# Optimization experiments

Measured on AMD Instinct MI355X. Metric: run time of the kernel, lower is better.

The kernel has to match this reference:

```python
import jax, jax.numpy as jnp
import numpy as np

B, S, DIM = 2, 2048, 2048
N_HEADS, N_KV_HEADS, HEAD_DIM = 16, 4, 128
ROPE_THETA = 10000.0
N_REP = N_HEADS // N_KV_HEADS


def make_freq_cis(seq_len, head_dim, theta):
    # (seq_len, head_dim//2, 2, 2) rotation matrices [[cos,-sin],[sin,cos]]
    freqs = 1.0 / (theta ** (np.arange(0, head_dim, 2, dtype=np.float32) / head_dim))
    t = np.arange(seq_len, dtype=np.float32)
    ang = np.outer(t, freqs)  # [S, head_dim//2]
    cos, sin = np.cos(ang), np.sin(ang)
    row0 = np.stack([cos, -sin], axis=-1)
    row1 = np.stack([sin, cos], axis=-1)
    return jnp.asarray(np.stack([row0, row1], axis=-2))  # [S, hd/2, 2, 2]


def setup_inputs() -> dict:
    key = jax.random.key(0)
    ks = jax.random.split(key, 5)
    std = DIM ** -0.5
    x = jax.random.normal(ks[0], (B, S, DIM), dtype=jnp.float32)
    wq = jax.random.normal(ks[1], (N_HEADS * HEAD_DIM, DIM), dtype=jnp.float32) * std
    wk = jax.random.normal(ks[2], (N_KV_HEADS * HEAD_DIM, DIM), dtype=jnp.float32) * std
    wv = jax.random.normal(ks[3], (N_KV_HEADS * HEAD_DIM, DIM), dtype=jnp.float32) * std
    wo = jax.random.normal(ks[4], (DIM, N_HEADS * HEAD_DIM), dtype=jnp.float32) * std
    freq_cis = make_freq_cis(S, HEAD_DIM, ROPE_THETA)
    return {"x": x, "freq_cis": freq_cis, "wq": wq, "wk": wk, "wv": wv, "wo": wo}


def apply_rotary(xh, fc):
    # xh: [B,S,H,hd]; fc: [S, hd/2, 2, 2]
    b, s, h, hd = xh.shape
    xr = xh.reshape(b, s, h, hd // 2, 2)
    out = jnp.einsum('bshdj,sdij->bshdi', xr, fc)
    return out.reshape(b, s, h, hd)


def attention_fwd(x, freq_cis, wq, wk, wv, wo):
    b, s, _ = x.shape
    xq = (x @ wq.T).reshape(b, s, N_HEADS, HEAD_DIM)
    xk = (x @ wk.T).reshape(b, s, N_KV_HEADS, HEAD_DIM)
    xv = (x @ wv.T).reshape(b, s, N_KV_HEADS, HEAD_DIM)
    xq = apply_rotary(xq, freq_cis[:s])
    xk = apply_rotary(xk, freq_cis[:s])
    # GQA repeat_kv (repeat_interleave along head dim)
    xk = jnp.repeat(xk, N_REP, axis=2)
    xv = jnp.repeat(xv, N_REP, axis=2)
    scale = HEAD_DIM ** -0.5
    scores = jnp.einsum('bqhd,bkhd->bhqk', xq, xk) * scale
    causal = jnp.tril(jnp.ones((s, s), dtype=bool))
    scores = jnp.where(causal[None, None], scores, jnp.float32(-1e30))
    probs = jax.nn.softmax(scores, axis=-1)
    out = jnp.einsum('bhqk,bkhd->bqhd', probs, xv).reshape(b, s, N_HEADS * HEAD_DIM)
    return out @ wo.T


def reference(x, freq_cis, wq, wk, wv, wo):
    return attention_fwd(x, freq_cis, wq, wk, wv, wo)
```

## Files before the change

kernel.cpp:

```cpp
#include <hip/hip_runtime.h>

#define S_LEN 2048
#define N_B 2
#define N_H 16
#define N_KVH 4
#define HD 128
#define LDQ 2048
#define LDK 1024

typedef __bf16 bf16x8 __attribute__((ext_vector_type(8)));
typedef float f32x4 __attribute__((ext_vector_type(4)));
typedef float f32x16 __attribute__((ext_vector_type(16)));
typedef int v2i __attribute__((ext_vector_type(2)));

__device__ __forceinline__ float bf2f(unsigned short u){
  unsigned int x = ((unsigned int)u) << 16; float f;
  __builtin_memcpy(&f, &x, 4); return f;
}
__device__ __forceinline__ unsigned short f2bf(float f){
  unsigned int x; __builtin_memcpy(&x, &f, 4);
  unsigned int r = x + 0x7fff + ((x >> 16) & 1);
  return (unsigned short)(r >> 16);
}
__device__ __forceinline__ unsigned int cvt_pk_bf16(float lo, float hi){
  unsigned int u;
  asm("v_cvt_pk_bf16_f32 %0, %1, %2" : "=v"(u) : "v"(lo), "v"(hi));
  return u;
}
__device__ __forceinline__ void gload16(const void* g, void* l){
  __builtin_amdgcn_global_load_lds((const __attribute__((address_space(1))) void*)g,
                                   (__attribute__((address_space(3))) void*)l, 16, 0, 0);
}

__global__ void cast_all(const float* __restrict__ x,  const float* __restrict__ wq,
                         const float* __restrict__ wk, const float* __restrict__ wv,
                         const float* __restrict__ wo, unsigned short* __restrict__ xb,
                         unsigned short* __restrict__ wqb, unsigned short* __restrict__ wkb,
                         unsigned short* __restrict__ wvb, unsigned short* __restrict__ wob){
  int i = blockIdx.x * 256 + threadIdx.x;
  const float* in; unsigned short* out; int j;
  if (i < 1048576)      { in = x;  out = xb;  j = i; }
  else if (i < 1572864) { in = wq; out = wqb; j = i - 1048576; }
  else if (i < 1703936) { in = wk; out = wkb; j = i - 1572864; }
  else if (i < 1835008) { in = wv; out = wvb; j = i - 1703936; }
  else                  { in = wo; out = wob; j = i - 1835008; }
  const float4* p = (const float4*)in + (size_t)j * 2;
  float4 a = p[0], b = p[1];
  uint4 o;
  o.x = (unsigned)f2bf(a.x) | ((unsigned)f2bf(a.y) << 16);
  o.y = (unsigned)f2bf(a.z) | ((unsigned)f2bf(a.w) << 16);
  o.z = (unsigned)f2bf(b.x) | ((unsigned)f2bf(b.y) << 16);
  o.w = (unsigned)f2bf(b.z) | ((unsigned)f2bf(b.w) << 16);
  ((uint4*)out)[j] = o;
}

__global__ void rope_kernel(unsigned short* __restrict__ X, const float* __restrict__ FC,
                            int cpr_log2, int ld_log2, int n8){
  int i = blockIdx.x * 256 + threadIdx.x;
  if (i >= n8) return;
  int row = i >> cpr_log2;
  int col = (i & ((1 << cpr_log2) - 1)) << 3;
  size_t idx = ((size_t)row << ld_log2) + col;
  int s = row & (S_LEN - 1);
  int d = col & (HD - 1);
  uint4 v = *(const uint4*)(X + idx);
  unsigned short* pv = (unsigned short*)&v;
  const float4* f4 = (const float4*)FC + ((size_t)s * 64 + (d >> 1));
  uint4 ov; unsigned short* po = (unsigned short*)&ov;
#pragma unroll
  for (int p = 0; p < 4; p++){
    float4 f = f4[p];
    float e = bf2f(pv[2*p]), o = bf2f(pv[2*p+1]);
    po[2*p]   = f2bf(f.x * e + f.y * o);
    po[2*p+1] = f2bf(f.z * e + f.w * o);
  }
  *(uint4*)(X + idx) = ov;
}

__global__ void transpose_v(const unsigned short* __restrict__ V, unsigned short* __restrict__ Vt, int ld){
  __shared__ unsigned short tile[32][33];
  int t = threadIdx.x;
  int s0 = blockIdx.x * 32;
  int c0 = blockIdx.y * 32;
  int r = t >> 3, cg = (t & 7) * 4;
  uint2 in2 = *(const uint2*)(V + (size_t)(s0 + r) * ld + c0 + cg);
  unsigned short* pi = (unsigned short*)&in2;
  tile[r][cg+0] = pi[0]; tile[r][cg+1] = pi[1]; tile[r][cg+2] = pi[2]; tile[r][cg+3] = pi[3];
  __syncthreads();
  int b = s0 >> 11, sl = s0 & (S_LEN - 1);
  int kvh = c0 >> 7, dd0 = c0 & (HD - 1);
  int dd = t >> 3, sg = (t & 7) * 4;
  uint2 o2; unsigned short* po = (unsigned short*)&o2;
  po[0] = tile[sg+0][dd]; po[1] = tile[sg+1][dd]; po[2] = tile[sg+2][dd]; po[3] = tile[sg+3][dd];
  *(uint2*)(Vt + (size_t)((b * N_KVH + kvh) * HD + dd0 + dd) * S_LEN + sl + sg) = o2;
}

__device__ __forceinline__ void storeC(float* C, size_t idx, float v){ C[idx] = v; }
__device__ __forceinline__ void storeC(unsigned short* C, size_t idx, float v){ C[idx] = f2bf(v); }

template <typename OutT>
__global__ __launch_bounds__(256, 2) void gemm_nt(const unsigned short* __restrict__ A,
                                                  const unsigned short* __restrict__ Bm,
                                                  OutT* __restrict__ C,
                                                  int M, int N, int K, int nbn){
  extern __shared__ char smem[];
  char* sA = smem; char* sB = smem + 16384;
  int bid = blockIdx.x;
  bid = (bid & 7) * (gridDim.x >> 3) + (bid >> 3);
  int bn = bid % nbn, bm = bid / nbn;
  int row0 = bm * 128, col0 = bn * 128;
  int t = threadIdx.x; int w = t >> 6, l = t & 63;
  int lr = l & 15, lg = l >> 4;
  int srow = t >> 3;
  int sg = (t & 7) ^ (srow & 7);
  const unsigned short* agp = A + (size_t)(row0 + srow) * K + sg * 8;
  const unsigned short* bgp = Bm + (size_t)(col0 + srow) * K + sg * 8;
  int wr = w >> 1, wc = w & 1;
  f32x4 acc[4][4] = {};
  for (int k0 = 0; k0 < K; k0 += 64){
    __syncthreads();
#pragma unroll
    for (int i = 0; i < 4; i++){
      gload16(agp + (size_t)i * 32 * K + k0, sA + i * 4096 + w * 1024);
      gload16(bgp + (size_t)i * 32 * K + k0, sB + i * 4096 + w * 1024);
    }
    __syncthreads();
#pragma unroll
    for (int kk = 0; kk < 2; kk++){
      bf16x8 af[4], bfv[4];
#pragma unroll
      for (int m = 0; m < 4; m++){
        int row = wr * 64 + m * 16 + lr;
        int kg = kk * 4 + lg;
        af[m] = *(const bf16x8*)(sA + row * 128 + ((kg ^ (row & 7)) << 4));
      }
#pragma unroll
      for (int n = 0; n < 4; n++){
        int row = wc * 64 + n * 16 + lr;
        int kg = kk * 4 + lg;
        bfv[n] = *(const bf16x8*)(sB + row * 128 + ((kg ^ (row & 7)) << 4));
      }
#pragma unroll
      for (int m = 0; m < 4; m++)
#pragma unroll
        for (int n = 0; n < 4; n++)
          acc[m][n] = __builtin_amdgcn_mfma_f32_16x16x32_bf16(af[m], bfv[n], acc[m][n], 0, 0, 0);
    }
  }
#pragma unroll
  for (int m = 0; m < 4; m++)
#pragma unroll
    for (int n = 0; n < 4; n++)
#pragma unroll
      for (int r = 0; r < 4; r++){
        int rr = row0 + wr * 64 + m * 16 + lg * 4 + r;
        int cc = col0 + wc * 64 + n * 16 + lr;
        storeC(C, (size_t)rr * N + cc, acc[m][n][r]);
      }
}

template <typename OutT>
__global__ __launch_bounds__(512, 2) void gemm_tpl(const unsigned short* __restrict__ A,
                                                   const unsigned short* __restrict__ Bm,
                                                   OutT* __restrict__ C,
                                                   int M, int N, int K, int nbn){
  extern __shared__ char smem[];
  int bid = blockIdx.x;
  bid = (bid & 7) * (gridDim.x >> 3) + (bid >> 3);
  int bn = bid % nbn, bm = bid / nbn;
  int row0 = bm * 128, col0 = bn * 256;
  int t = threadIdx.x, w = t >> 6, l = t & 63;
  int lr = l & 15, lg = l >> 4;
  int wm = w >> 2, wn = w & 3;
  int srow = t >> 3;
  int sg = (t & 7) ^ (srow & 7);
  const unsigned short* agp = A + (size_t)(row0 + srow) * K + sg * 8;
  const unsigned short* bgp = Bm + (size_t)(col0 + srow) * K + sg * 8;
  int nk = K >> 6;
  f32x4 acc[4][4] = {};

#define TPL_STAGE(j, s) do {                                                   \
    char* base_ = smem + (s) * 49152;                                          \
    int k0_ = (j) << 6;                                                        \
    _Pragma("unroll")                                                          \
    for (int i_ = 0; i_ < 2; i_++)                                             \
      gload16(agp + (size_t)i_ * 64 * K + k0_, base_ + i_ * 8192 + w * 1024);  \
    _Pragma("unroll")                                                          \
    for (int i_ = 0; i_ < 4; i_++)                                             \
      gload16(bgp + (size_t)i_ * 64 * K + k0_, base_ + 16384 + i_ * 8192 + w * 1024); \
  } while(0)

  TPL_STAGE(0, 0);
  TPL_STAGE(1, 1);
  int slot = 0;
  for (int j = 0; j < nk; j++){
    if (j + 1 < nk) asm volatile("s_waitcnt vmcnt(6)" ::: "memory");
    else            asm volatile("s_waitcnt vmcnt(0)" ::: "memory");
    __builtin_amdgcn_s_barrier();
    asm volatile("" ::: "memory");
    char* sA = smem + slot * 49152;
    char* sB = sA + 16384;
    bf16x8 af[2][4], bf[2][4];
#pragma unroll
    for (int kk = 0; kk < 2; kk++){
#pragma unroll
      for (int m = 0; m < 4; m++){
        int row = wm * 64 + m * 16 + lr;
        int kg = kk * 4 + lg;
        af[kk][m] = *(const bf16x8*)(sA + row * 128 + ((kg ^ (row & 7)) << 4));
      }
#pragma unroll
      for (int n = 0; n < 4; n++){
        int row = wn * 64 + n * 16 + lr;
        int kg = kk * 4 + lg;
        bf[kk][n] = *(const bf16x8*)(sB + row * 128 + ((kg ^ (row & 7)) << 4));
      }
    }
    if (j + 2 < nk){
      int sn = slot + 2; if (sn >= 3) sn -= 3;
      TPL_STAGE(j + 2, sn);
    }
    __builtin_amdgcn_s_setprio(1);
#pragma unroll
    for (int kk = 0; kk < 2; kk++)
#pragma unroll
      for (int m = 0; m < 4; m++)
#pragma unroll
        for (int n = 0; n < 4; n++)
          acc[m][n] = __builtin_amdgcn_mfma_f32_16x16x32_bf16(af[kk][m], bf[kk][n], acc[m][n], 0, 0, 0);
    __builtin_amdgcn_s_setprio(0);
    slot++; if (slot == 3) slot = 0;
  }
#undef TPL_STAGE
#pragma unroll
  for (int m = 0; m < 4; m++)
#pragma unroll
    for (int n = 0; n < 4; n++)
#pragma unroll
      for (int r = 0; r < 4; r++){
        int rr = row0 + wm * 64 + m * 16 + lg * 4 + r;
        int cc = col0 + wn * 64 + n * 16 + lr;
        storeC(C, (size_t)rr * N + cc, acc[m][n][r]);
      }
}

__global__ __launch_bounds__(256, 2) void attn_fwd(const unsigned short* __restrict__ Q,
                                                   const unsigned short* __restrict__ Kb,
                                                   const unsigned short* __restrict__ Vt,
                                                   unsigned short* __restrict__ P0,
                                                   unsigned short* __restrict__ P1,
                                                   float2* __restrict__ ML){
  extern __shared__ char smem[];
  const float SOFT_C = 0.088388347648318447f * 1.4426950408889634f;
  const float THR_RAW = 62.0f;
  int bid = blockIdx.x;
  bid = ((bid & 7) << 6) | (bid >> 3);
  int slot = bid & 15, h = (bid >> 4) & 15, b = bid >> 8;
  int p = slot & 7, half = slot >> 3;
  int kvh = h >> 2;
  int t = threadIdx.x, w = t >> 6, l = t & 63;
  int lq = l & 31, lh = l >> 5;
  unsigned short* Pout = half ? P1 : P0;
  float2* mlb = ML + half * (N_B * S_LEN * N_H);

  int gA = (t & 15) ^ (t >> 4);
  const unsigned short* kgp = Kb + ((size_t)(b * S_LEN) + (t >> 4)) * LDK + kvh * HD + gA * 8;
  int gV = (t & 7) ^ ((t >> 3) & 7);
  const unsigned short* vgp = Vt + ((size_t)((b * N_KVH + kvh) * HD) + (t >> 3)) * S_LEN + gV * 8;

  for (int phase = 0; phase < 2; phase++){
    int qt = phase ? (15 - p) : p;
    int q_lane = qt * 128 + w * 32 + lq;
    const unsigned short* qbase = Q + ((size_t)(b * S_LEN + q_lane)) * LDQ + h * HD + lh * 8;
    bf16x8 qf[8];
#pragma unroll
    for (int ks = 0; ks < 8; ks++)
      qf[ks] = *(const bf16x8*)(qbase + ks * 16);

    f32x16 o_acc[4] = {};
    float m_run = -1e4f, l_run = 0.f;
    int t_begin = half ? (qt + 1) : 0;
    int t_end   = half ? (2 * qt + 2) : (qt + 1);

    int pk0 = t_begin * 64;
#pragma unroll
    for (int m = 0; m < 4; m++)
      gload16(kgp + (size_t)(pk0 + m * 16) * LDK, smem + m * 4096 + w * 1024);
#pragma unroll
    for (int i = 0; i < 4; i++)
      gload16(vgp + (size_t)i * 32 * S_LEN + pk0, smem + 16384 + i * 4096 + w * 1024);
    __syncthreads();

    int cur = 0;
    for (int tix = t_begin; tix < t_end; tix++){
      int k0 = tix * 64;
      char* sK = smem + (cur << 15);
      char* sV = sK + 16384;
      if (tix + 1 < t_end){
        char* nb = smem + ((cur ^ 1) << 15);
        int nk0 = k0 + 64;
#pragma unroll
        for (int m = 0; m < 4; m++)
          gload16(kgp + (size_t)(nk0 + m * 16) * LDK, nb + m * 4096 + w * 1024);
#pragma unroll
        for (int i = 0; i < 4; i++)
          gload16(vgp + (size_t)i * 32 * S_LEN + nk0, nb + 16384 + i * 4096 + w * 1024);
      }

      f32x16 sc[2] = {};
      __builtin_amdgcn_s_setprio(1);
#pragma unroll
      for (int ks = 0; ks < 8; ks++){
#pragma unroll
        for (int n = 0; n < 2; n++){
          int row = n * 32 + lq;
          int pg = (ks * 2 + lh) ^ (row & 15);
          bf16x8 kf = *(const bf16x8*)(sK + row * 256 + pg * 16);
          sc[n] = __builtin_amdgcn_mfma_f32_32x32x16_bf16(kf, qf[ks], sc[n], 0, 0, 0);
        }
      }
      __builtin_amdgcn_s_setprio(0);
      if (tix >= 2 * qt){
#pragma unroll
        for (int n = 0; n < 2; n++)
#pragma unroll
          for (int reg = 0; reg < 16; reg++){
            int kv = k0 + n * 32 + (reg & 3) + 8 * (reg >> 2) + 4 * lh;
            if (kv > q_lane) sc[n][reg] = -1e30f;
          }
      }
      float tmax = sc[0][0];
#pragma unroll
      for (int n = 0; n < 2; n++)
#pragma unroll
        for (int reg = 0; reg < 16; reg++) tmax = fmaxf(tmax, sc[n][reg]);
      tmax = fmaxf(tmax, __shfl_xor(tmax, 32));
      if (!__all(tmax - m_run <= THR_RAW)){
        float nm = fmaxf(m_run, tmax);
        float rs = exp2f((m_run - nm) * SOFT_C);
        m_run = nm;
        l_run *= rs;
#pragma unroll
        for (int n = 0; n < 4; n++)
#pragma unroll
          for (int j = 0; j < 16; j++) o_acc[n][j] *= rs;
      }
      float lsum = 0.f;
#pragma unroll
      for (int n = 0; n < 2; n++)
#pragma unroll
        for (int reg = 0; reg < 16; reg++){
          float pv = exp2f((sc[n][reg] - m_run) * SOFT_C);
          sc[n][reg] = pv;
          lsum += pv;
        }
      lsum += __shfl_xor(lsum, 32);
      l_run += lsum;

      bf16x8 pb[4];
#pragma unroll
      for (int ks = 0; ks < 4; ks++){
        int n = ks >> 1;
        int R0 = (2 * ks) & 3, R1 = (2 * ks + 1) & 3;
        unsigned int WA0 = cvt_pk_bf16(sc[n][4 * R0 + 0], sc[n][4 * R0 + 1]);
        unsigned int WA1 = cvt_pk_bf16(sc[n][4 * R0 + 2], sc[n][4 * R0 + 3]);
        unsigned int WB0 = cvt_pk_bf16(sc[n][4 * R1 + 0], sc[n][4 * R1 + 1]);
        unsigned int WB1 = cvt_pk_bf16(sc[n][4 * R1 + 2], sc[n][4 * R1 + 3]);
        v2i s0 = __builtin_amdgcn_permlane32_swap((int)WA0, (int)WB0, false, false);
        v2i s1 = __builtin_amdgcn_permlane32_swap((int)WA1, (int)WB1, false, false);
        unsigned int pu[4] = {(unsigned int)s0.x, (unsigned int)s1.x,
                              (unsigned int)s0.y, (unsigned int)s1.y};
        pb[ks] = *(bf16x8*)pu;
      }
      __builtin_amdgcn_s_setprio(1);
#pragma unroll
      for (int n = 0; n < 4; n++){
#pragma unroll
        for (int ks = 0; ks < 4; ks++){
          int row = n * 32 + lq;
          int pg = (ks * 2 + lh) ^ (row & 7);
          bf16x8 vf = *(const bf16x8*)(sV + row * 128 + pg * 16);
          o_acc[n] = __builtin_amdgcn_mfma_f32_32x32x16_bf16(vf, pb[ks], o_acc[n], 0, 0, 0);
        }
      }
      __builtin_amdgcn_s_setprio(0);
      __syncthreads();
      cur ^= 1;
    }
    unsigned short* ob = Pout + ((size_t)(b * S_LEN + q_lane)) * LDQ + h * HD + 4 * lh;
#pragma unroll
    for (int n = 0; n < 4; n++)
#pragma unroll
      for (int g = 0; g < 4; g++){
        unsigned int u0 = cvt_pk_bf16(o_acc[n][4 * g + 0], o_acc[n][4 * g + 1]);
        unsigned int u1 = cvt_pk_bf16(o_acc[n][4 * g + 2], o_acc[n][4 * g + 3]);
        uint2 o2; o2.x = u0; o2.y = u1;
        *(uint2*)(ob + n * 32 + g * 8) = o2;
      }
    if (lh == 0)
      mlb[(size_t)(b * S_LEN + q_lane) * N_H + h] = make_float2(m_run, l_run);
  }
}

__global__ void attn_merge(unsigned short* __restrict__ P0, const unsigned short* __restrict__ P1,
                           const float2* __restrict__ ML){
  const float SOFT_C = 0.088388347648318447f * 1.4426950408889634f;
  int tid = blockIdx.x * 256 + threadIdx.x;
  float2 a = ML[tid >> 4];
  float2 c = ML[(N_B * S_LEN * N_H) + (tid >> 4)];
  float m = fmaxf(a.x, c.x);
  float w0 = exp2f((a.x - m) * SOFT_C) * a.y;
  float w1 = exp2f((c.x - m) * SOFT_C) * c.y;
  float inv = 1.0f / (w0 + w1);
  float s0 = exp2f((a.x - m) * SOFT_C) * inv;
  float s1 = exp2f((c.x - m) * SOFT_C) * inv;
  uint4 u0 = *(const uint4*)(P0 + (size_t)tid * 8);
  uint4 u1 = *(const uint4*)(P1 + (size_t)tid * 8);
  unsigned short* q0 = (unsigned short*)&u0;
  unsigned short* q1 = (unsigned short*)&u1;
  uint4 o;
  unsigned int* po = (unsigned int*)&o;
#pragma unroll
  for (int j = 0; j < 4; j++){
    float lo = s0 * bf2f(q0[2*j])   + s1 * bf2f(q1[2*j]);
    float hi = s0 * bf2f(q0[2*j+1]) + s1 * bf2f(q1[2*j+1]);
    po[j] = cvt_pk_bf16(lo, hi);
  }
  *(uint4*)(P0 + (size_t)tid * 8) = o;
}

extern "C" void kernel_launch(void* const* d_in, const int* in_sizes, int n_in,
                              void* d_out, int out_size, void* d_ws, size_t ws_size,
                              hipStream_t stream) {
  const float* x  = (const float*)d_in[0];
  const float* fc = (const float*)d_in[1];
  const float* wq = (const float*)d_in[2];
  const float* wk = (const float*)d_in[3];
  const float* wv = (const float*)d_in[4];
  const float* wo = (const float*)d_in[5];
  float* out = (float*)d_out;

  char* ws = (char*)d_ws;
  unsigned short* xb  = (unsigned short*)(ws);
  unsigned short* wqb = (unsigned short*)(ws + 16777216);
  unsigned short* wkb = (unsigned short*)(ws + 25165824);
  unsigned short* wvb = (unsigned short*)(ws + 27262976);
  unsigned short* wob = (unsigned short*)(ws + 29360128);
  unsigned short* qb_ = (unsigned short*)(ws + 37748736);
  unsigned short* kvb = (unsigned short*)(ws + 54525952);
  unsigned short* vtb = (unsigned short*)(ws + 62914560);
  unsigned short* ab_ = (unsigned short*)(ws + 67108864);
  unsigned short* p1_ = xb;
  float2*         ml_ = (float2*)wqb;

  cast_all<<<9216, 256, 0, stream>>>(x, wq, wk, wv, wo, xb, wqb, wkb, wvb, wob);

  gemm_tpl<unsigned short><<<256, 512, 147456, stream>>>(xb, wqb, qb_, 4096, 2048, 2048, 8);
  gemm_nt<unsigned short><<<256, 256, 32768, stream>>>(xb, wkb, kvb, 4096, 1024, 2048, 8);

  rope_kernel<<<4096, 256, 0, stream>>>(qb_, fc, 8, 11, 1048576);
  rope_kernel<<<1024, 256, 0, stream>>>(kvb, fc, 6, 10, 262144);

  transpose_v<<<dim3(128, 16), 256, 0, stream>>>(kvb + 512, vtb, 1024);

  attn_fwd<<<512, 256, 65536, stream>>>(qb_, kvb, vtb, ab_, p1_, ml_);
  attn_merge<<<4096, 256, 0, stream>>>(ab_, p1_, ml_);

  gemm_tpl<float><<<256, 512, 147456, stream>>>(ab_, wob, out, 4096, 2048, 2048, 8);
}
```

Measured before the change: 207.4 us.

## Stage attention K/V tiles through registers with new LDS layout; merge rope launches

The attention kernel stops using direct global-to-LDS loads. It now loads the next K/V tile into registers before the QK MFMAs and writes it to the other LDS buffer after the PV MFMAs. The LDS layout and XOR swizzle are redesigned so fragment reads use precomputed per-lane offsets. Separately, the two RoPE launches (Q and K) are fused into one kernel to save a launch. The register staging adds VGPR pressure and may lower occupancy.

```diff
diff --git a/kernel.cpp b/kernel.cpp
--- a/kernel.cpp
+++ b/kernel.cpp
@@ -54,16 +54,15 @@
   ((uint4*)out)[j] = o;
 }
 
-__global__ void rope_kernel(unsigned short* __restrict__ X, const float* __restrict__ FC,
-                            int cpr_log2, int ld_log2, int n8){
+__global__ void rope_both(unsigned short* __restrict__ Qb, unsigned short* __restrict__ KV,
+                          const float* __restrict__ FC){
   int i = blockIdx.x * 256 + threadIdx.x;
-  if (i >= n8) return;
-  int row = i >> cpr_log2;
-  int col = (i & ((1 << cpr_log2) - 1)) << 3;
-  size_t idx = ((size_t)row << ld_log2) + col;
+  unsigned short* X; int row, col;
+  if (i < 1048576){ row = i >> 8; col = (i & 255) << 3; X = Qb + (((size_t)row) << 11) + col; }
+  else { int j = i - 1048576; row = j >> 6; col = (j & 63) << 3; X = KV + (((size_t)row) << 10) + col; }
   int s = row & (S_LEN - 1);
   int d = col & (HD - 1);
-  uint4 v = *(const uint4*)(X + idx);
+  uint4 v = *(const uint4*)X;
   unsigned short* pv = (unsigned short*)&v;
   const float4* f4 = (const float4*)FC + ((size_t)s * 64 + (d >> 1));
   uint4 ov; unsigned short* po = (unsigned short*)&ov;
@@ -74,7 +73,7 @@
     po[2*p]   = f2bf(f.x * e + f.y * o);
     po[2*p+1] = f2bf(f.z * e + f.w * o);
   }
-  *(uint4*)(X + idx) = ov;
+  *(uint4*)X = ov;
 }
 
 __global__ void transpose_v(const unsigned short* __restrict__ V, unsigned short* __restrict__ Vt, int ld){
@@ -263,10 +262,13 @@
   unsigned short* Pout = half ? P1 : P0;
   float2* mlb = ML + half * (N_B * S_LEN * N_H);
 
-  int gA = (t & 15) ^ (t >> 4);
-  const unsigned short* kgp = Kb + ((size_t)(b * S_LEN) + (t >> 4)) * LDK + kvh * HD + gA * 8;
-  int gV = (t & 7) ^ ((t >> 3) & 7);
-  const unsigned short* vgp = Vt + ((size_t)((b * N_KVH + kvh) * HD) + (t >> 3)) * S_LEN + gV * 8;
+  const unsigned short* kg0 = Kb + ((size_t)(b * S_LEN) + (t >> 4)) * LDK + kvh * HD + (t & 15) * 8;
+  const unsigned short* vg0 = Vt + ((size_t)((b * N_KVH + kvh) * HD) + (t >> 3)) * S_LEN + (t & 7) * 8;
+  int kwbase = (t & 15) * 1024 + (((t >> 4) ^ (t & 7)) << 4);
+  int vwbase = (t & 7) * 2048 + (((t >> 3) ^ (t & 7)) << 4);
+  int la[4];
+#pragma unroll
+  for (int j = 0; j < 4; j++) la[j] = (lq ^ (2 * j + lh)) << 4;
 
   for (int phase = 0; phase < 2; phase++){
     int qt = phase ? (15 - p) : p;
@@ -282,29 +284,35 @@
     int t_begin = half ? (qt + 1) : 0;
     int t_end   = half ? (2 * qt + 2) : (qt + 1);
 
-    int pk0 = t_begin * 64;
-#pragma unroll
-    for (int m = 0; m < 4; m++)
-      gload16(kgp + (size_t)(pk0 + m * 16) * LDK, smem + m * 4096 + w * 1024);
-#pragma unroll
-    for (int i = 0; i < 4; i++)
-      gload16(vgp + (size_t)i * 32 * S_LEN + pk0, smem + 16384 + i * 4096 + w * 1024);
+    {
+      int k0 = t_begin * 64;
+      uint4 kr[4], vr[4];
+#pragma unroll
+      for (int i = 0; i < 4; i++){
+        kr[i] = *(const uint4*)(kg0 + (size_t)(k0 + 16 * i) * LDK);
+        vr[i] = *(const uint4*)(vg0 + k0 + (size_t)i * 32 * S_LEN);
+      }
+#pragma unroll
+      for (int i = 0; i < 4; i++){
+        *(uint4*)(smem + kwbase + i * 256) = kr[i];
+        *(uint4*)(smem + 16384 + vwbase + i * 512) = vr[i];
+      }
+    }
     __syncthreads();
 
     int cur = 0;
     for (int tix = t_begin; tix < t_end; tix++){
       int k0 = tix * 64;
-      char* sK = smem + (cur << 15);
-      char* sV = sK + 16384;
-      if (tix + 1 < t_end){
-        char* nb = smem + ((cur ^ 1) << 15);
+      char* kb = smem + (cur << 15);
+      uint4 kr[4], vr[4];
+      bool have_next = (tix + 1 < t_end);
+      if (have_next){
         int nk0 = k0 + 64;
 #pragma unroll
-        for (int m = 0; m < 4; m++)
-          gload16(kgp + (size_t)(nk0 + m * 16) * LDK, nb + m * 4096 + w * 1024);
-#pragma unroll
-        for (int i = 0; i < 4; i++)
-          gload16(vgp + (size_t)i * 32 * S_LEN + nk0, nb + 16384 + i * 4096 + w * 1024);
+        for (int i = 0; i < 4; i++){
+          kr[i] = *(const uint4*)(kg0 + (size_t)(nk0 + 16 * i) * LDK);
+          vr[i] = *(const uint4*)(vg0 + nk0 + (size_t)i * 32 * S_LEN);
+        }
       }
 
       f32x16 sc[2] = {};
@@ -313,9 +321,7 @@
       for (int ks = 0; ks < 8; ks++){
 #pragma unroll
         for (int n = 0; n < 2; n++){
-          int row = n * 32 + lq;
-          int pg = (ks * 2 + lh) ^ (row & 15);
-          bf16x8 kf = *(const bf16x8*)(sK + row * 256 + pg * 16);
+          bf16x8 kf = *(const bf16x8*)(kb + lh * 1024 + ks * 2048 + n * 512 + la[ks & 3]);
           sc[n] = __builtin_amdgcn_mfma_f32_32x32x16_bf16(kf, qf[ks], sc[n], 0, 0, 0);
         }
       }
@@ -377,13 +383,19 @@
       for (int n = 0; n < 4; n++){
 #pragma unroll
         for (int ks = 0; ks < 4; ks++){
-          int row = n * 32 + lq;
-          int pg = (ks * 2 + lh) ^ (row & 7);
-          bf16x8 vf = *(const bf16x8*)(sV + row * 128 + pg * 16);
+          bf16x8 vf = *(const bf16x8*)(kb + 16384 + lh * 2048 + ks * 4096 + n * 512 + la[ks]);
           o_acc[n] = __builtin_amdgcn_mfma_f32_32x32x16_bf16(vf, pb[ks], o_acc[n], 0, 0, 0);
         }
       }
       __builtin_amdgcn_s_setprio(0);
+      if (have_next){
+        char* nb = smem + ((cur ^ 1) << 15);
+#pragma unroll
+        for (int i = 0; i < 4; i++){
+          *(uint4*)(nb + kwbase + i * 256) = kr[i];
+          *(uint4*)(nb + 16384 + vwbase + i * 512) = vr[i];
+        }
+      }
       __syncthreads();
       cur ^= 1;
     }
@@ -458,8 +470,7 @@
   gemm_tpl<unsigned short><<<256, 512, 147456, stream>>>(xb, wqb, qb_, 4096, 2048, 2048, 8);
   gemm_nt<unsigned short><<<256, 256, 32768, stream>>>(xb, wkb, kvb, 4096, 1024, 2048, 8);
 
-  rope_kernel<<<4096, 256, 0, stream>>>(qb_, fc, 8, 11, 1048576);
-  rope_kernel<<<1024, 256, 0, stream>>>(kvb, fc, 6, 10, 262144);
+  rope_both<<<5120, 256, 0, stream>>>(qb_, kvb, fc);
 
   transpose_v<<<dim3(128, 16), 256, 0, stream>>>(kvb + 512, vtb, 1024);
 
```

New measurement: 246.5 us. +18.9%, slower.

## Fuse Q/K/V projections into one GEMM with transposed V epilogue, merge RoPE launches

Applied to the files above, without the earlier changes.

Replaces the separate Q GEMM and KV GEMM with a single triple-buffered 128x256 GEMM over the concatenated wq/wk/wv weights. Its epilogue writes Q, K (now a 512-wide buffer), and V directly in transposed layout, which removes the transpose_v kernel. The two RoPE launches become one kernel covering both Q and K. The fused GEMM depends on wqb, wkb and wvb sitting contiguously in the workspace so they act as one 3072-row weight matrix. It also writes V with strided 8-byte stores into the transposed buffer, which may coalesce less well.

```diff
diff --git a/kernel.cpp b/kernel.cpp
--- a/kernel.cpp
+++ b/kernel.cpp
@@ -6,7 +6,7 @@
 #define N_KVH 4
 #define HD 128
 #define LDQ 2048
-#define LDK 1024
+#define LDK 512
 
 typedef __bf16 bf16x8 __attribute__((ext_vector_type(8)));
 typedef float f32x4 __attribute__((ext_vector_type(4)));
@@ -54,16 +54,15 @@
   ((uint4*)out)[j] = o;
 }
 
-__global__ void rope_kernel(unsigned short* __restrict__ X, const float* __restrict__ FC,
-                            int cpr_log2, int ld_log2, int n8){
+__global__ void rope_both(unsigned short* __restrict__ Qb, unsigned short* __restrict__ Kbuf,
+                          const float* __restrict__ FC){
   int i = blockIdx.x * 256 + threadIdx.x;
-  if (i >= n8) return;
-  int row = i >> cpr_log2;
-  int col = (i & ((1 << cpr_log2) - 1)) << 3;
-  size_t idx = ((size_t)row << ld_log2) + col;
+  unsigned short* X; int row, col;
+  if (i < 1048576){ row = i >> 8; col = (i & 255) << 3; X = Qb + (((size_t)row) << 11) + col; }
+  else { int j = i - 1048576; row = j >> 6; col = (j & 63) << 3; X = Kbuf + (((size_t)row) << 9) + col; }
   int s = row & (S_LEN - 1);
   int d = col & (HD - 1);
-  uint4 v = *(const uint4*)(X + idx);
+  uint4 v = *(const uint4*)X;
   unsigned short* pv = (unsigned short*)&v;
   const float4* f4 = (const float4*)FC + ((size_t)s * 64 + (d >> 1));
   uint4 ov; unsigned short* po = (unsigned short*)&ov;
@@ -74,89 +73,123 @@
     po[2*p]   = f2bf(f.x * e + f.y * o);
     po[2*p+1] = f2bf(f.z * e + f.w * o);
   }
-  *(uint4*)(X + idx) = ov;
-}
-
-__global__ void transpose_v(const unsigned short* __restrict__ V, unsigned short* __restrict__ Vt, int ld){
-  __shared__ unsigned short tile[32][33];
-  int t = threadIdx.x;
-  int s0 = blockIdx.x * 32;
-  int c0 = blockIdx.y * 32;
-  int r = t >> 3, cg = (t & 7) * 4;
-  uint2 in2 = *(const uint2*)(V + (size_t)(s0 + r) * ld + c0 + cg);
-  unsigned short* pi = (unsigned short*)&in2;
-  tile[r][cg+0] = pi[0]; tile[r][cg+1] = pi[1]; tile[r][cg+2] = pi[2]; tile[r][cg+3] = pi[3];
-  __syncthreads();
-  int b = s0 >> 11, sl = s0 & (S_LEN - 1);
-  int kvh = c0 >> 7, dd0 = c0 & (HD - 1);
-  int dd = t >> 3, sg = (t & 7) * 4;
-  uint2 o2; unsigned short* po = (unsigned short*)&o2;
-  po[0] = tile[sg+0][dd]; po[1] = tile[sg+1][dd]; po[2] = tile[sg+2][dd]; po[3] = tile[sg+3][dd];
-  *(uint2*)(Vt + (size_t)((b * N_KVH + kvh) * HD + dd0 + dd) * S_LEN + sl + sg) = o2;
+  *(uint4*)X = ov;
 }
 
 __device__ __forceinline__ void storeC(float* C, size_t idx, float v){ C[idx] = v; }
 __device__ __forceinline__ void storeC(unsigned short* C, size_t idx, float v){ C[idx] = f2bf(v); }
 
-template <typename OutT>
-__global__ __launch_bounds__(256, 2) void gemm_nt(const unsigned short* __restrict__ A,
-                                                  const unsigned short* __restrict__ Bm,
-                                                  OutT* __restrict__ C,
-                                                  int M, int N, int K, int nbn){
+__global__ __launch_bounds__(512, 2) void gemm_qkv(const unsigned short* __restrict__ A,
+                                                   const unsigned short* __restrict__ Bm,
+                                                   unsigned short* __restrict__ Qo,
+                                                   unsigned short* __restrict__ Ko,
+                                                   unsigned short* __restrict__ Vt){
   extern __shared__ char smem[];
-  char* sA = smem; char* sB = smem + 16384;
+  const int K = 2048;
   int bid = blockIdx.x;
-  bid = (bid & 7) * (gridDim.x >> 3) + (bid >> 3);
-  int bn = bid % nbn, bm = bid / nbn;
-  int row0 = bm * 128, col0 = bn * 128;
-  int t = threadIdx.x; int w = t >> 6, l = t & 63;
+  bid = (bid & 7) * 48 + (bid >> 3);
+  int bn = bid % 12, bm = bid / 12;
+  int row0 = bm * 128, col0 = bn * 256;
+  int t = threadIdx.x, w = t >> 6, l = t & 63;
   int lr = l & 15, lg = l >> 4;
+  int wm = w >> 2, wn = w & 3;
   int srow = t >> 3;
   int sg = (t & 7) ^ (srow & 7);
   const unsigned short* agp = A + (size_t)(row0 + srow) * K + sg * 8;
   const unsigned short* bgp = Bm + (size_t)(col0 + srow) * K + sg * 8;
-  int wr = w >> 1, wc = w & 1;
+  int nk = K >> 6;
   f32x4 acc[4][4] = {};
-  for (int k0 = 0; k0 < K; k0 += 64){
-    __syncthreads();
-#pragma unroll
-    for (int i = 0; i < 4; i++){
-      gload16(agp + (size_t)i * 32 * K + k0, sA + i * 4096 + w * 1024);
-      gload16(bgp + (size_t)i * 32 * K + k0, sB + i * 4096 + w * 1024);
+
+#define TPL_STAGE(j, s) do {                                                   \
+    char* base_ = smem + (s) * 49152;                                          \
+    int k0_ = (j) << 6;                                                        \
+    _Pragma("unroll")                                                          \
+    for (int i_ = 0; i_ < 2; i_++)                                             \
+      gload16(agp + (size_t)i_ * 64 * K + k0_, base_ + i_ * 8192 + w * 1024);  \
+    _Pragma("unroll")                                                          \
+    for (int i_ = 0; i_ < 4; i_++)                                             \
+      gload16(bgp + (size_t)i_ * 64 * K + k0_, base_ + 16384 + i_ * 8192 + w * 1024); \
+  } while(0)
+
+  TPL_STAGE(0, 0);
+  TPL_STAGE(1, 1);
+  int slot = 0;
+  for (int j = 0; j < nk; j++){
+    if (j + 1 < nk) asm volatile("s_waitcnt vmcnt(6)" ::: "memory");
+    else            asm volatile("s_waitcnt vmcnt(0)" ::: "memory");
+    __builtin_amdgcn_s_barrier();
+    asm volatile("" ::: "memory");
+    char* sA = smem + slot * 49152;
+    char* sB = sA + 16384;
+    bf16x8 af[2][4], bf[2][4];
+#pragma unroll
+    for (int kk = 0; kk < 2; kk++){
+#pragma unroll
+      for (int m = 0; m < 4; m++){
+        int row = wm * 64 + m * 16 + lr;
+        int kg = kk * 4 + lg;
+        af[kk][m] = *(const bf16x8*)(sA + row * 128 + ((kg ^ (row & 7)) << 4));
+      }
+#pragma unroll
+      for (int n = 0; n < 4; n++){
+        int row = wn * 64 + n * 16 + lr;
+        int kg = kk * 4 + lg;
+        bf[kk][n] = *(const bf16x8*)(sB + row * 128 + ((kg ^ (row & 7)) << 4));
+      }
     }
-    __syncthreads();
-#pragma unroll
-    for (int kk = 0; kk < 2; kk++){
-      bf16x8 af[4], bfv[4];
-#pragma unroll
-      for (int m = 0; m < 4; m++){
-        int row = wr * 64 + m * 16 + lr;
-        int kg = kk * 4 + lg;
-        af[m] = *(const bf16x8*)(sA + row * 128 + ((kg ^ (row & 7)) << 4));
-      }
+    if (j + 2 < nk){
+      int sn = slot + 2; if (sn >= 3) sn -= 3;
+      TPL_STAGE(j + 2, sn);
+    }
+    __builtin_amdgcn_s_setprio(1);
+#pragma unroll
+    for (int kk = 0; kk < 2; kk++)
+#pragma unroll
+      for (int m = 0; m < 4; m++)
+#pragma unroll
+        for (int n = 0; n < 4; n++)
+          acc[m][n] = __builtin_amdgcn_mfma_f32_16x16x32_bf16(af[kk][m], bf[kk][n], acc[m][n], 0, 0, 0);
+    __builtin_amdgcn_s_setprio(0);
+    slot++; if (slot == 3) slot = 0;
+  }
+#undef TPL_STAGE
+  if (col0 < 2048){
+#pragma unroll
+    for (int m = 0; m < 4; m++)
+#pragma unroll
+      for (int n = 0; n < 4; n++)
+#pragma unroll
+        for (int r = 0; r < 4; r++){
+          int rr = row0 + wm * 64 + m * 16 + lg * 4 + r;
+          int cc = col0 + wn * 64 + n * 16 + lr;
+          Qo[(size_t)rr * 2048 + cc] = f2bf(acc[m][n][r]);
+        }
+  } else if (col0 < 2560){
+#pragma unroll
+    for (int m = 0; m < 4; m++)
+#pragma unroll
+      for (int n = 0; n < 4; n++)
+#pragma unroll
+        for (int r = 0; r < 4; r++){
+          int rr = row0 + wm * 64 + m * 16 + lg * 4 + r;
+          int cc = col0 - 2048 + wn * 64 + n * 16 + lr;
+          Ko[(size_t)rr * 512 + cc] = f2bf(acc[m][n][r]);
+        }
+  } else {
+#pragma unroll
+    for (int m = 0; m < 4; m++)
 #pragma unroll
       for (int n = 0; n < 4; n++){
-        int row = wc * 64 + n * 16 + lr;
-        int kg = kk * 4 + lg;
-        bfv[n] = *(const bf16x8*)(sB + row * 128 + ((kg ^ (row & 7)) << 4));
-      }
-#pragma unroll
-      for (int m = 0; m < 4; m++)
-#pragma unroll
-        for (int n = 0; n < 4; n++)
-          acc[m][n] = __builtin_amdgcn_mfma_f32_16x16x32_bf16(af[m], bfv[n], acc[m][n], 0, 0, 0);
-    }
-  }
-#pragma unroll
-  for (int m = 0; m < 4; m++)
-#pragma unroll
-    for (int n = 0; n < 4; n++)
-#pragma unroll
-      for (int r = 0; r < 4; r++){
-        int rr = row0 + wr * 64 + m * 16 + lg * 4 + r;
-        int cc = col0 + wc * 64 + n * 16 + lr;
-        storeC(C, (size_t)rr * N + cc, acc[m][n][r]);
-      }
+        int vcol = col0 - 2560 + wn * 64 + n * 16 + lr;
+        int kvh = vcol >> 7, d = vcol & (HD - 1);
+        int s0 = row0 + wm * 64 + m * 16 + lg * 4;
+        int bb = s0 >> 11, sl = s0 & (S_LEN - 1);
+        uint2 o2;
+        o2.x = cvt_pk_bf16(acc[m][n][0], acc[m][n][1]);
+        o2.y = cvt_pk_bf16(acc[m][n][2], acc[m][n][3]);
+        *(uint2*)(Vt + ((size_t)((bb * N_KVH + kvh) * HD + d)) * S_LEN + sl) = o2;
+      }
+  }
 }
 
 template <typename OutT>
@@ -447,7 +480,7 @@
   unsigned short* wvb = (unsigned short*)(ws + 27262976);
   unsigned short* wob = (unsigned short*)(ws + 29360128);
   unsigned short* qb_ = (unsigned short*)(ws + 37748736);
-  unsigned short* kvb = (unsigned short*)(ws + 54525952);
+  unsigned short* kb_ = (unsigned short*)(ws + 54525952);
   unsigned short* vtb = (unsigned short*)(ws + 62914560);
   unsigned short* ab_ = (unsigned short*)(ws + 67108864);
   unsigned short* p1_ = xb;
@@ -455,15 +488,11 @@
 
   cast_all<<<9216, 256, 0, stream>>>(x, wq, wk, wv, wo, xb, wqb, wkb, wvb, wob);
 
-  gemm_tpl<unsigned short><<<256, 512, 147456, stream>>>(xb, wqb, qb_, 4096, 2048, 2048, 8);
-  gemm_nt<unsigned short><<<256, 256, 32768, stream>>>(xb, wkb, kvb, 4096, 1024, 2048, 8);
-
-  rope_kernel<<<4096, 256, 0, stream>>>(qb_, fc, 8, 11, 1048576);
-  rope_kernel<<<1024, 256, 0, stream>>>(kvb, fc, 6, 10, 262144);
-
-  transpose_v<<<dim3(128, 16), 256, 0, stream>>>(kvb + 512, vtb, 1024);
-
-  attn_fwd<<<512, 256, 65536, stream>>>(qb_, kvb, vtb, ab_, p1_, ml_);
+  gemm_qkv<<<384, 512, 147456, stream>>>(xb, wqb, qb_, kb_, vtb);
+
+  rope_both<<<5120, 256, 0, stream>>>(qb_, kb_, fc);
+
+  attn_fwd<<<512, 256, 65536, stream>>>(qb_, kb_, vtb, ab_, p1_, ml_);
   attn_merge<<<4096, 256, 0, stream>>>(ab_, p1_, ml_);
 
   gemm_tpl<float><<<256, 512, 147456, stream>>>(ab_, wob, out, 4096, 2048, 2048, 8);
```

Result: faster. 194.5 us (median of 3 runs) (-6.2%).

## Fuse V transpose into KV GEMM epilogue and merge RoPE launches

Applied to the files above, without the earlier changes.

The KV projection GEMM now writes K into its own 512-wide buffer and writes V directly in transposed [b,kvh,d,s] layout from the epilogue. This removes the separate transpose kernel and its extra pass over V through global memory. The two RoPE launches are merged into one kernel that handles both Q and K. The transposed V stores write four consecutive sequence elements per lane, so those stores are strided and may coalesce poorly. LDK changes to 512 so the attention kernel reads the new K layout.

```diff
diff --git a/kernel.cpp b/kernel.cpp
--- a/kernel.cpp
+++ b/kernel.cpp
@@ -6,7 +6,7 @@
 #define N_KVH 4
 #define HD 128
 #define LDQ 2048
-#define LDK 1024
+#define LDK 512
 
 typedef __bf16 bf16x8 __attribute__((ext_vector_type(8)));
 typedef float f32x4 __attribute__((ext_vector_type(4)));
@@ -54,16 +54,15 @@
   ((uint4*)out)[j] = o;
 }
 
-__global__ void rope_kernel(unsigned short* __restrict__ X, const float* __restrict__ FC,
-                            int cpr_log2, int ld_log2, int n8){
+__global__ void rope_both(unsigned short* __restrict__ Qb, unsigned short* __restrict__ Kbuf,
+                          const float* __restrict__ FC){
   int i = blockIdx.x * 256 + threadIdx.x;
-  if (i >= n8) return;
-  int row = i >> cpr_log2;
-  int col = (i & ((1 << cpr_log2) - 1)) << 3;
-  size_t idx = ((size_t)row << ld_log2) + col;
+  unsigned short* X; int row, col;
+  if (i < 1048576){ row = i >> 8; col = (i & 255) << 3; X = Qb + (((size_t)row) << 11) + col; }
+  else { int j = i - 1048576; row = j >> 6; col = (j & 63) << 3; X = Kbuf + (((size_t)row) << 9) + col; }
   int s = row & (S_LEN - 1);
   int d = col & (HD - 1);
-  uint4 v = *(const uint4*)(X + idx);
+  uint4 v = *(const uint4*)X;
   unsigned short* pv = (unsigned short*)&v;
   const float4* f4 = (const float4*)FC + ((size_t)s * 64 + (d >> 1));
   uint4 ov; unsigned short* po = (unsigned short*)&ov;
@@ -74,40 +73,22 @@
     po[2*p]   = f2bf(f.x * e + f.y * o);
     po[2*p+1] = f2bf(f.z * e + f.w * o);
   }
-  *(uint4*)(X + idx) = ov;
-}
-
-__global__ void transpose_v(const unsigned short* __restrict__ V, unsigned short* __restrict__ Vt, int ld){
-  __shared__ unsigned short tile[32][33];
-  int t = threadIdx.x;
-  int s0 = blockIdx.x * 32;
-  int c0 = blockIdx.y * 32;
-  int r = t >> 3, cg = (t & 7) * 4;
-  uint2 in2 = *(const uint2*)(V + (size_t)(s0 + r) * ld + c0 + cg);
-  unsigned short* pi = (unsigned short*)&in2;
-  tile[r][cg+0] = pi[0]; tile[r][cg+1] = pi[1]; tile[r][cg+2] = pi[2]; tile[r][cg+3] = pi[3];
-  __syncthreads();
-  int b = s0 >> 11, sl = s0 & (S_LEN - 1);
-  int kvh = c0 >> 7, dd0 = c0 & (HD - 1);
-  int dd = t >> 3, sg = (t & 7) * 4;
-  uint2 o2; unsigned short* po = (unsigned short*)&o2;
-  po[0] = tile[sg+0][dd]; po[1] = tile[sg+1][dd]; po[2] = tile[sg+2][dd]; po[3] = tile[sg+3][dd];
-  *(uint2*)(Vt + (size_t)((b * N_KVH + kvh) * HD + dd0 + dd) * S_LEN + sl + sg) = o2;
+  *(uint4*)X = ov;
 }
 
 __device__ __forceinline__ void storeC(float* C, size_t idx, float v){ C[idx] = v; }
 __device__ __forceinline__ void storeC(unsigned short* C, size_t idx, float v){ C[idx] = f2bf(v); }
 
-template <typename OutT>
-__global__ __launch_bounds__(256, 2) void gemm_nt(const unsigned short* __restrict__ A,
+__global__ __launch_bounds__(256, 2) void gemm_kv(const unsigned short* __restrict__ A,
                                                   const unsigned short* __restrict__ Bm,
-                                                  OutT* __restrict__ C,
-                                                  int M, int N, int K, int nbn){
+                                                  unsigned short* __restrict__ Ko,
+                                                  unsigned short* __restrict__ Vt){
   extern __shared__ char smem[];
   char* sA = smem; char* sB = smem + 16384;
+  const int K = 2048;
   int bid = blockIdx.x;
-  bid = (bid & 7) * (gridDim.x >> 3) + (bid >> 3);
-  int bn = bid % nbn, bm = bid / nbn;
+  bid = (bid & 7) * 32 + (bid >> 3);
+  int bn = bid % 8, bm = bid / 8;
   int row0 = bm * 128, col0 = bn * 128;
   int t = threadIdx.x; int w = t >> 6, l = t & 63;
   int lr = l & 15, lg = l >> 4;
@@ -147,16 +128,32 @@
           acc[m][n] = __builtin_amdgcn_mfma_f32_16x16x32_bf16(af[m], bfv[n], acc[m][n], 0, 0, 0);
     }
   }
-#pragma unroll
-  for (int m = 0; m < 4; m++)
-#pragma unroll
-    for (int n = 0; n < 4; n++)
-#pragma unroll
-      for (int r = 0; r < 4; r++){
-        int rr = row0 + wr * 64 + m * 16 + lg * 4 + r;
-        int cc = col0 + wc * 64 + n * 16 + lr;
-        storeC(C, (size_t)rr * N + cc, acc[m][n][r]);
-      }
+  if (col0 < 512){
+#pragma unroll
+    for (int m = 0; m < 4; m++)
+#pragma unroll
+      for (int n = 0; n < 4; n++)
+#pragma unroll
+        for (int r = 0; r < 4; r++){
+          int rr = row0 + wr * 64 + m * 16 + lg * 4 + r;
+          int cc = col0 + wc * 64 + n * 16 + lr;
+          Ko[(size_t)rr * 512 + cc] = f2bf(acc[m][n][r]);
+        }
+  } else {
+#pragma unroll
+    for (int m = 0; m < 4; m++)
+#pragma unroll
+      for (int n = 0; n < 4; n++){
+        int vcol = col0 - 512 + wc * 64 + n * 16 + lr;
+        int kvh = vcol >> 7, d = vcol & (HD - 1);
+        int s0 = row0 + wr * 64 + m * 16 + lg * 4;
+        int bb = s0 >> 11, sl = s0 & (S_LEN - 1);
+        uint2 o2;
+        o2.x = cvt_pk_bf16(acc[m][n][0], acc[m][n][1]);
+        o2.y = cvt_pk_bf16(acc[m][n][2], acc[m][n][3]);
+        *(uint2*)(Vt + ((size_t)((bb * N_KVH + kvh) * HD + d)) * S_LEN + sl) = o2;
+      }
+  }
 }
 
 template <typename OutT>
@@ -447,7 +444,7 @@
   unsigned short* wvb = (unsigned short*)(ws + 27262976);
   unsigned short* wob = (unsigned short*)(ws + 29360128);
   unsigned short* qb_ = (unsigned short*)(ws + 37748736);
-  unsigned short* kvb = (unsigned short*)(ws + 54525952);
+  unsigned short* kb_ = (unsigned short*)(ws + 54525952);
   unsigned short* vtb = (unsigned short*)(ws + 62914560);
   unsigned short* ab_ = (unsigned short*)(ws + 67108864);
   unsigned short* p1_ = xb;
@@ -456,14 +453,11 @@
   cast_all<<<9216, 256, 0, stream>>>(x, wq, wk, wv, wo, xb, wqb, wkb, wvb, wob);
 
   gemm_tpl<unsigned short><<<256, 512, 147456, stream>>>(xb, wqb, qb_, 4096, 2048, 2048, 8);
-  gemm_nt<unsigned short><<<256, 256, 32768, stream>>>(xb, wkb, kvb, 4096, 1024, 2048, 8);
-
-  rope_kernel<<<4096, 256, 0, stream>>>(qb_, fc, 8, 11, 1048576);
-  rope_kernel<<<1024, 256, 0, stream>>>(kvb, fc, 6, 10, 262144);
-
-  transpose_v<<<dim3(128, 16), 256, 0, stream>>>(kvb + 512, vtb, 1024);
-
-  attn_fwd<<<512, 256, 65536, stream>>>(qb_, kvb, vtb, ab_, p1_, ml_);
+  gemm_kv<<<256, 256, 32768, stream>>>(xb, wkb, kb_, vtb);
+
+  rope_both<<<5120, 256, 0, stream>>>(qb_, kb_, fc);
+
+  attn_fwd<<<512, 256, 65536, stream>>>(qb_, kb_, vtb, ab_, p1_, ml_);
   attn_merge<<<4096, 256, 0, stream>>>(ab_, p1_, ml_);
 
   gemm_tpl<float><<<256, 512, 147456, stream>>>(ab_, wob, out, 4096, 2048, 2048, 8);
```

After: 199.3 us. 1.04x faster.
